# Performance work log

Hardware: AMD Instinct MI355X
Metric: run time of the kernel (lower is better)

## Reference

```python
import jax, jax.numpy as jnp
import numpy as np

EPS = 0.001   # EPSILON2
T1 = 1.0
T2 = 100.0
DISC = 16     # number of discrete features
B, F, K1, K2 = 524288, 16, 16, 8


def _enforce(v):
    # Enforced autograd fn: forward = max(v, EPS), backward = identity (STE)
    return v + jax.lax.stop_gradient(jnp.maximum(v, EPS) - v)


def _soft_bin(cont, interval, i_min):
    """cont: [B,F]; interval: [F,K]; i_min: [F]. Vectorized over features/bins.
    Returns (STE one-hot out [B, F*K], kmeans_loss scalar)."""
    # bin centers = i_min + running cumsum of (enforced) gaps -> [F,K]
    centers = i_min[:, None] + jnp.cumsum(_enforce(interval), axis=1)
    d = (cont[:, :, None] - centers[None, :, :]) ** 2          # [B,F,K]
    s1 = jax.nn.softmax(-T1 * d, axis=-1)                      # kmeans softmax
    kmeans_loss = jnp.sum(jnp.mean(jnp.sum(d * s1, axis=-1), axis=0))
    s2 = jax.nn.softmax(-T2 * d, axis=-1)                      # sharp softmax
    oh = jax.nn.one_hot(jnp.argmax(s2, axis=-1), d.shape[-1], dtype=s2.dtype)
    out = s2 + jax.lax.stop_gradient(oh - s2)                  # STE one-hot
    return out.reshape(cont.shape[0], -1), kmeans_loss


def setup_inputs() -> dict:
    key = jax.random.key(0)
    k1, k2, k3 = jax.random.split(key, 3)
    x = jax.random.uniform(k1, (B, DISC + F), dtype=jnp.float32)
    interval = jax.random.uniform(k2, (F, K1), dtype=jnp.float32,
                                  minval=0.01, maxval=0.12)
    interval2 = jax.random.uniform(k3, (F, K2), dtype=jnp.float32,
                                   minval=0.02, maxval=0.2)
    i_min = jnp.zeros((F,), dtype=jnp.float32)
    return {"x": x, "interval": interval, "interval2": interval2, "i_min": i_min}


def reference(x, interval, interval2, i_min):
    x_disc, cont = x[:, :DISC], x[:, DISC:]
    out1, loss1 = _soft_bin(cont, interval, i_min)
    out2, loss2 = _soft_bin(cont, interval2, i_min)
    total_out = jnp.concatenate([x_disc, out1, out2], axis=1)  # [B, DISC+F*(K1+K2)]
    return total_out, loss1 + loss2
```

## Files before the change

### kernel.cpp

```cpp
#include <hip/hip_runtime.h>


constexpr int kB      = 524288;
constexpr int kF      = 16;
constexpr int kK1     = 16;
constexpr int kK2     = 8;
constexpr int kRowIn  = 32;
constexpr int kRowOut = 400;
constexpr float kEps  = 0.001f;
constexpr int kTPB    = 256;
constexpr int kGrid   = kB / kTPB;
constexpr int kC4     = kRowOut / 4;
constexpr int kXStride = 33;
constexpr int kWPB    = kTPB / 64;

typedef float f32x4 __attribute__((ext_vector_type(4)));

template <int K>
__device__ __forceinline__ int soft_argmax_loss(const float* __restrict__ dd,
                                                double& lacc)
{
#pragma clang fp contract(off)
    float se = 0.f, sde = 0.f;
#pragma unroll
    for (int k = 0; k < K; ++k) {
        float e = __expf(-dd[k]);
        se += e; sde += dd[k] * e;
    }
    lacc += (double)(sde / se);

    float z[K];
#pragma unroll
    for (int k = 0; k < K; ++k) z[k] = -100.0f * dd[k];
    float m = z[0]; int kmax = 0;
#pragma unroll
    for (int k = 1; k < K; ++k) {
        if (z[k] > m) { m = z[k]; kmax = k; }
    }

    bool cand = false;
#pragma unroll
    for (int k = 0; k < K; ++k)
        cand |= (k < kmax) & (z[k] >= m - 2.4e-7f);
    if (cand) {
        float e2[K]; float ss = 0.f;
        for (int k = 0; k < K; ++k) { e2[k] = expf(z[k] - m); ss += e2[k]; }
        int km = 0; float pmax = e2[0] / ss;
        for (int k = 1; k < K; ++k) {
            float p = e2[k] / ss;
            if (p > pmax) { pmax = p; km = k; }
        }
        kmax = km;
    }
    return kmax;
}

__global__ __launch_bounds__(kTPB) void binlayer_main(
    const float* __restrict__ x,
    const float* __restrict__ interval,
    const float* __restrict__ interval2,
    const float* __restrict__ i_min,
    float* __restrict__ out,
    double* __restrict__ partial,
    int perwave)
{
#pragma clang fp contract(off)
    __shared__ float sC1[kF][kK1];
    __shared__ float sC2[kF][kK2];
    __shared__ float sX[kTPB * kXStride];
    __shared__ unsigned char sIdx[kTPB * kF];
    __shared__ double sL[kWPB];

    const int tid = threadIdx.x;
    const int w   = tid >> 6;
    const int l   = tid & 63;

    if (tid < kF) {
        const float base = i_min[tid];
        float run = 0.f;
        for (int k = 0; k < kK1; ++k) {
            run += fmaxf(interval[tid * kK1 + k], kEps);
            sC1[tid][k] = base + run;
        }
        run = 0.f;
        for (int k = 0; k < kK2; ++k) {
            run += fmaxf(interval2[tid * kK2 + k], kEps);
            sC2[tid][k] = base + run;
        }
    }
    __syncthreads();

    const long long rowBase = (long long)blockIdx.x * kTPB;
    const int R0 = w * 64;

    const f32x4* __restrict__ xin4 = (const f32x4*)(x + (rowBase + R0) * kRowIn);
#pragma unroll
    for (int i = 0; i < 8; ++i) {
        int flat = i * 64 + l;
        f32x4 v = xin4[flat];
        int r = R0 + (flat >> 3), c4 = flat & 7;
        float* p = &sX[r * kXStride + c4 * 4];
        p[0] = v.x; p[1] = v.y; p[2] = v.z; p[3] = v.w;
    }
    asm volatile("s_waitcnt lgkmcnt(0)" ::: "memory");

    double lacc = 0.0;
    const float* __restrict__ myc = &sX[tid * kXStride + 16];

#pragma unroll 1
    for (int f = 0; f < kF; ++f) {
        const float c = myc[f];

        float dd1[kK1];
#pragma unroll
        for (int k = 0; k < kK1; ++k) { float t = c - sC1[f][k]; dd1[k] = t * t; }
        int k1 = soft_argmax_loss<kK1>(dd1, lacc);

        float dd2[kK2];
#pragma unroll
        for (int k = 0; k < kK2; ++k) { float t = c - sC2[f][k]; dd2[k] = t * t; }
        int k2 = soft_argmax_loss<kK2>(dd2, lacc);

        sIdx[tid * kF + f] = (unsigned char)(k1 | (k2 << 4));
    }
    asm volatile("s_waitcnt lgkmcnt(0)" ::: "memory");

#pragma unroll
    for (int off = 32; off > 0; off >>= 1) lacc += __shfl_down(lacc, off);
    if (perwave) {
        if (l == 0) partial[(long long)blockIdx.x * kWPB + w] = lacc;
    } else {
        if (l == 0) sL[w] = lacc;
        __syncthreads();
        if (tid == 0) partial[blockIdx.x] = sL[0] + sL[1] + sL[2] + sL[3];
    }

    f32x4* __restrict__ o4 = (f32x4*)(out + (rowBase + R0) * kRowOut);
#pragma unroll 1
    for (int i = 0; i < kC4; ++i) {
        unsigned idx = (unsigned)(i * 64 + l);
        unsigned r = idx / 100u;
        unsigned c = idx - r * 100u;
        unsigned rr = (unsigned)R0 + r;
        f32x4 o;
        if (c < 4u) {
            const float* p = &sX[rr * kXStride + c * 4u];
            o.x = p[0]; o.y = p[1]; o.z = p[2]; o.w = p[3];
        } else if (c < 68u) {
            unsigned u = c - 4u, f = u >> 2, q = (u & 3u) * 4u;
            unsigned k = sIdx[rr * kF + f] & 15u;
            o.x = (k == q + 0u) ? 1.f : 0.f;
            o.y = (k == q + 1u) ? 1.f : 0.f;
            o.z = (k == q + 2u) ? 1.f : 0.f;
            o.w = (k == q + 3u) ? 1.f : 0.f;
        } else {
            unsigned u = c - 68u, f = u >> 1, q = (u & 1u) * 4u;
            unsigned k = (unsigned)(sIdx[rr * kF + f]) >> 4;
            o.x = (k == q + 0u) ? 1.f : 0.f;
            o.y = (k == q + 1u) ? 1.f : 0.f;
            o.z = (k == q + 2u) ? 1.f : 0.f;
            o.w = (k == q + 3u) ? 1.f : 0.f;
        }
        __builtin_nontemporal_store(o, &o4[idx]);
    }
}

__global__ __launch_bounds__(256) void binlayer_finalize(
    const double* __restrict__ partial,
    float* __restrict__ out,
    int n)
{
    __shared__ double sL[4];
    const int tid = threadIdx.x;
    double s = 0.0;
    for (int i = tid; i < n; i += 256)
        s += partial[i];
#pragma unroll
    for (int off = 32; off > 0; off >>= 1) s += __shfl_down(s, off);
    if ((tid & 63) == 0) sL[tid >> 6] = s;
    __syncthreads();
    if (tid == 0)
        out[(long long)kB * kRowOut] =
            (float)((sL[0] + sL[1] + sL[2] + sL[3]) * (1.0 / (double)kB));
}

extern "C" void kernel_launch(void* const* d_in, const int* in_sizes, int n_in,
                              void* d_out, int out_size, void* d_ws, size_t ws_size,
                              hipStream_t stream)
{
    const float* x    = (const float*)d_in[0];
    const float* itv1 = (const float*)d_in[1];
    const float* itv2 = (const float*)d_in[2];
    const float* imin = (const float*)d_in[3];
    float* out = (float*)d_out;
    double* partial = (double*)d_ws;

    const int perwave = (ws_size >= (size_t)kGrid * kWPB * sizeof(double)) ? 1 : 0;
    const int nPartial = perwave ? kGrid * kWPB : kGrid;

    binlayer_main<<<kGrid, kTPB, 0, stream>>>(x, itv1, itv2, imin, out, partial, perwave);
    binlayer_finalize<<<1, 256, 0, stream>>>(partial, out, nPartial);
}
```

Measured before the change: 911.5 us.

## Interleave output stores with compute in feature groups of four

The kernel now writes the passthrough columns right after staging and splits the feature loop into four groups. Each group's one-hot output columns are stored immediately after that group's bin indices are computed, so global writes overlap with later compute instead of running as one tail phase. The stores switch from nontemporal to regular stores, and each wave now writes scattered 16-byte chunks within rows rather than fully contiguous spans, which may hurt write coalescing and cache behaviour.

```diff
diff --git a/kernel.cpp b/kernel.cpp
--- a/kernel.cpp
+++ b/kernel.cpp
@@ -10,7 +10,6 @@
 constexpr float kEps  = 0.001f;
 constexpr int kTPB    = 256;
 constexpr int kGrid   = kB / kTPB;
-constexpr int kC4     = kRowOut / 4;
 constexpr int kXStride = 33;
 constexpr int kWPB    = kTPB / 64;
 
@@ -55,6 +54,16 @@
     return kmax;
 }
 
+__device__ __forceinline__ f32x4 onehot4(unsigned k, unsigned q)
+{
+    f32x4 o;
+    o.x = (k == q + 0u) ? 1.f : 0.f;
+    o.y = (k == q + 1u) ? 1.f : 0.f;
+    o.z = (k == q + 2u) ? 1.f : 0.f;
+    o.w = (k == q + 3u) ? 1.f : 0.f;
+    return o;
+}
+
 __global__ __launch_bounds__(kTPB) void binlayer_main(
     const float* __restrict__ x,
     const float* __restrict__ interval,
@@ -104,26 +113,62 @@
     }
     asm volatile("s_waitcnt lgkmcnt(0)" ::: "memory");
 
+    f32x4* __restrict__ o4 = (f32x4*)(out + (rowBase + R0) * kRowOut);
+
+#pragma unroll
+    for (int it = 0; it < 4; ++it) {
+        unsigned idx = (unsigned)(it * 64 + l);
+        unsigned rr = idx >> 2, c = idx & 3u;
+        const float* p = &sX[(R0 + rr) * kXStride + c * 4u];
+        f32x4 o; o.x = p[0]; o.y = p[1]; o.z = p[2]; o.w = p[3];
+        o4[rr * 100u + c] = o;
+    }
+
     double lacc = 0.0;
     const float* __restrict__ myc = &sX[tid * kXStride + 16];
 
 #pragma unroll 1
-    for (int f = 0; f < kF; ++f) {
-        const float c = myc[f];
-
-        float dd1[kK1];
-#pragma unroll
-        for (int k = 0; k < kK1; ++k) { float t = c - sC1[f][k]; dd1[k] = t * t; }
-        int k1 = soft_argmax_loss<kK1>(dd1, lacc);
-
-        float dd2[kK2];
-#pragma unroll
-        for (int k = 0; k < kK2; ++k) { float t = c - sC2[f][k]; dd2[k] = t * t; }
-        int k2 = soft_argmax_loss<kK2>(dd2, lacc);
-
-        sIdx[tid * kF + f] = (unsigned char)(k1 | (k2 << 4));
-    }
-    asm volatile("s_waitcnt lgkmcnt(0)" ::: "memory");
+    for (int g = 0; g < 4; ++g) {
+#pragma unroll 1
+        for (int fl = 0; fl < 4; ++fl) {
+            const int f = g * 4 + fl;
+            const float c = myc[f];
+
+            float dd1[kK1];
+#pragma unroll
+            for (int k = 0; k < kK1; ++k) { float t = c - sC1[f][k]; dd1[k] = t * t; }
+            int k1 = soft_argmax_loss<kK1>(dd1, lacc);
+
+            float dd2[kK2];
+#pragma unroll
+            for (int k = 0; k < kK2; ++k) { float t = c - sC2[f][k]; dd2[k] = t * t; }
+            int k2 = soft_argmax_loss<kK2>(dd2, lacc);
+
+            sIdx[tid * kF + f] = (unsigned char)(k1 | (k2 << 4));
+        }
+        asm volatile("s_waitcnt lgkmcnt(0)" ::: "memory");
+
+#pragma unroll 1
+        for (int it = 0; it < 24; ++it) {
+            unsigned idx = (unsigned)(it * 64 + l);
+            unsigned rr = idx / 24u;
+            unsigned j  = idx - rr * 24u;
+            unsigned c, q, k;
+            if (j < 16u) {
+                unsigned f = (unsigned)(g * 4) + (j >> 2);
+                c = 4u + 4u * f + (j & 3u);
+                q = (j & 3u) * 4u;
+                k = sIdx[(R0 + rr) * kF + f] & 15u;
+            } else {
+                unsigned jj = j - 16u;
+                unsigned f = (unsigned)(g * 4) + (jj >> 1);
+                c = 68u + 2u * f + (jj & 1u);
+                q = (jj & 1u) * 4u;
+                k = (unsigned)(sIdx[(R0 + rr) * kF + f]) >> 4;
+            }
+            o4[rr * 100u + c] = onehot4(k, q);
+        }
+    }
 
 #pragma unroll
     for (int off = 32; off > 0; off >>= 1) lacc += __shfl_down(lacc, off);
@@ -134,35 +179,6 @@
         __syncthreads();
         if (tid == 0) partial[blockIdx.x] = sL[0] + sL[1] + sL[2] + sL[3];
     }
-
-    f32x4* __restrict__ o4 = (f32x4*)(out + (rowBase + R0) * kRowOut);
-#pragma unroll 1
-    for (int i = 0; i < kC4; ++i) {
-        unsigned idx = (unsigned)(i * 64 + l);
-        unsigned r = idx / 100u;
-        unsigned c = idx - r * 100u;
-        unsigned rr = (unsigned)R0 + r;
-        f32x4 o;
-        if (c < 4u) {
-            const float* p = &sX[rr * kXStride + c * 4u];
-            o.x = p[0]; o.y = p[1]; o.z = p[2]; o.w = p[3];
-        } else if (c < 68u) {
-            unsigned u = c - 4u, f = u >> 2, q = (u & 3u) * 4u;
-            unsigned k = sIdx[rr * kF + f] & 15u;
-            o.x = (k == q + 0u) ? 1.f : 0.f;
-            o.y = (k == q + 1u) ? 1.f : 0.f;
-            o.z = (k == q + 2u) ? 1.f : 0.f;
-            o.w = (k == q + 3u) ? 1.f : 0.f;
-        } else {
-            unsigned u = c - 68u, f = u >> 1, q = (u & 1u) * 4u;
-            unsigned k = (unsigned)(sIdx[rr * kF + f]) >> 4;
-            o.x = (k == q + 0u) ? 1.f : 0.f;
-            o.y = (k == q + 1u) ? 1.f : 0.f;
-            o.z = (k == q + 2u) ? 1.f : 0.f;
-            o.w = (k == q + 3u) ? 1.f : 0.f;
-        }
-        __builtin_nontemporal_store(o, &o4[idx]);
-    }
 }
 
 __global__ __launch_bounds__(256) void binlayer_finalize(
```

Measured after the change: 1.003 ms. +10.0%, slower.
